# Optimization experiments

Hardware: AMD Instinct MI355X
Metric: run time of the kernel (lower is better)

## Reference

```python
import jax, jax.numpy as jnp
import numpy as np

NEG_INF = -1e6  # d2l masked_softmax fill value


def setup_inputs() -> dict:
    key = jax.random.key(0)
    kq, kk, kv, kl = jax.random.split(key, 4)
    n, s, d = 32, 2048, 64
    queries = jax.random.normal(kq, (n, s, d), dtype=jnp.float32)
    keys = jax.random.normal(kk, (n, s, d), dtype=jnp.float32)
    values = jax.random.normal(kv, (n, s, d), dtype=jnp.float32)
    valid_lens = jax.random.randint(kl, (n,), 1, s + 1, dtype=jnp.int32)
    return {"queries": queries, "keys": keys, "values": values, "valid_lens": valid_lens}


def reference(queries, keys, values, valid_lens):
    d = queries.shape[-1]
    # scores: [n, q, k]
    scores = jnp.einsum("nqd,nkd->nqk", queries, keys) / jnp.sqrt(jnp.float32(d))
    kv_len = scores.shape[-1]
    # masked_softmax: positions >= valid_len get NEG_INF before softmax
    mask = jnp.arange(kv_len, dtype=jnp.int32)[None, None, :] < valid_lens[:, None, None]
    scores = jnp.where(mask, scores, NEG_INF)
    attn = jax.nn.softmax(scores, axis=-1)
    # dropout rate 0.0 (inference) -> identity
    return jnp.einsum("nqk,nkd->nqd", attn, values)
```

## Files before the change

### kernel.cpp

```cpp
#include <hip/hip_runtime.h>
#include <hip/hip_bf16.h>


typedef short bf16x8 __attribute__((ext_vector_type(8)));
typedef float f32x4  __attribute__((ext_vector_type(4)));
typedef unsigned int u32;
typedef u32 u32x2 __attribute__((ext_vector_type(2)));
typedef u32 u32x4 __attribute__((ext_vector_type(4)));

#define SEQ 2048
#define DH 64
#define BK 64
#define LDSP 72
#define SCLQ 0.18033688011112042f

static __device__ __forceinline__ short f2bf(float f) {
    unsigned u = __float_as_uint(f);
    return (short)((u + 0x7FFFu + ((u >> 16) & 1u)) >> 16);
}
static __device__ __forceinline__ u32 pk2bf(float lo, float hi) {
    __hip_bfloat162 h = __float22bfloat162_rn(float2{lo, hi});
    return *(u32*)&h;
}

__global__ __launch_bounds__(256, 4)
void prepass(const float* __restrict__ K, const float* __restrict__ V,
             short* __restrict__ Kbf, short* __restrict__ Vt)
{
    __shared__ short T[DH][LDSP];

    const int tid  = threadIdx.x;
    const int wave = tid >> 6;
    const int lane = tid & 63;
    const int b  = blockIdx.x & 31;
    const int kt = blockIdx.x >> 5;
    const int k0 = kt * BK;
    const size_t bo = (size_t)b * SEQ * DH;

    const float* Ks = K + bo + (size_t)k0 * DH;
    u32* Kd = (u32*)(Kbf + bo + (size_t)k0 * DH);
    #pragma unroll
    for (int h = 0; h < 2; ++h) {
        const int c2 = tid + h * 256;
        f32x4 a = *(const f32x4*)(Ks + c2 * 8);
        f32x4 c = *(const f32x4*)(Ks + c2 * 8 + 4);
        u32x4 o;
        o[0] = pk2bf(a[0], a[1]); o[1] = pk2bf(a[2], a[3]);
        o[2] = pk2bf(c[0], c[1]); o[3] = pk2bf(c[2], c[3]);
        *(u32x4*)(Kd + c2 * 4) = o;
    }

    #pragma unroll
    for (int h = 0; h < 2; ++h) {
        const int d0 = wave * 8 + h * 32;
        const float* src = V + bo + (size_t)(k0 + lane) * DH + d0;
        f32x4 va = *(const f32x4*)(src);
        f32x4 vb = *(const f32x4*)(src + 4);
        #pragma unroll
        for (int j = 0; j < 4; ++j) {
            T[d0 + j][lane]     = f2bf(va[j]);
            T[d0 + 4 + j][lane] = f2bf(vb[j]);
        }
    }
    __syncthreads();

    short* Vd = Vt + (size_t)b * DH * SEQ;
    #pragma unroll
    for (int h = 0; h < 2; ++h) {
        const int c2 = tid + h * 256;
        const int d  = c2 >> 3;
        const int kc = (c2 & 7) * 8;
        *(bf16x8*)(Vd + (size_t)d * SEQ + k0 + kc) = *(const bf16x8*)(&T[d][kc]);
    }
}

template <bool PRE>
__global__ __launch_bounds__(256, 4)
void attn_fwd(const float* __restrict__ Q,
              const float* __restrict__ Kf, const float* __restrict__ Vf,
              const short* __restrict__ Kbf, const short* __restrict__ Vtg,
              const int* __restrict__ VL, float* __restrict__ O)
{
    __shared__ short Klds[BK][LDSP];
    __shared__ short Vt[DH][LDSP];
    __shared__ short Pw[4][16][LDSP];
    __shared__ int   Rsort[32];

    const int tid  = threadIdx.x;
    const int wave = tid >> 6;
    const int lane = tid & 63;
    const int g    = lane >> 4;
    const int l15  = lane & 15;

    if (tid < 32) {
        const int nv = (VL[tid] + BK - 1) >> 6;
        int rank = 0;
        for (int jj = 0; jj < 32; ++jj) {
            const int nj = (VL[jj] + BK - 1) >> 6;
            rank += (nj > nv) || (nj == nv && jj < tid);
        }
        Rsort[rank] = tid;
    }
    __syncthreads();

    const int jb = blockIdx.x & 255;
    const int sl = blockIdx.x >> 8;
    const int c8 = jb >> 5;
    const int qt = jb & 31;
    const int rk = (sl == 0) ? c8 : (sl == 1) ? (15 - c8)
                 : (sl == 2) ? (16 + c8) : (31 - c8);
    const int b  = Rsort[rk];

    const int vl  = VL[b];
    const int nkt = (vl + BK - 1) >> 6;

    const size_t bo = (size_t)b * SEQ * DH;
    const short* Kb = Kbf + bo;
    const short* Vb = Vtg + (size_t)b * DH * SEQ;
    const float* Kbf32 = Kf + bo;
    const float* Vbf32 = Vf + bo;

    const int qrow = qt * 64 + wave * 16 + l15;
    bf16x8 aq0, aq1;
    {
        const float* qp = Q + bo + (size_t)qrow * DH + g * 8;
        f32x4 q0 = *(const f32x4*)(qp);
        f32x4 q1 = *(const f32x4*)(qp + 4);
        f32x4 q2 = *(const f32x4*)(qp + 32);
        f32x4 q3 = *(const f32x4*)(qp + 36);
        #pragma unroll
        for (int j = 0; j < 4; ++j) {
            aq0[j]     = f2bf(q0[j] * SCLQ);
            aq0[j + 4] = f2bf(q1[j] * SCLQ);
            aq1[j]     = f2bf(q2[j] * SCLQ);
            aq1[j + 4] = f2bf(q3[j] * SCLQ);
        }
    }

    bf16x8 ones;
    #pragma unroll
    for (int j = 0; j < 8; ++j) ones[j] = (short)0x3F80;

    f32x4 oacc[4];
    #pragma unroll
    for (int i = 0; i < 4; ++i) oacc[i] = f32x4{0.f, 0.f, 0.f, 0.f};
    f32x4 lacc = f32x4{0.f, 0.f, 0.f, 0.f};

    bf16x8 kpre[2], vpre[2];
    f32x4 kpre32[4], vpre32[4];
    if (PRE) {
        #pragma unroll
        for (int h = 0; h < 2; ++h) {
            const int c2 = tid + h * 256;
            kpre[h] = *(const bf16x8*)(Kb + c2 * 8);
            vpre[h] = *(const bf16x8*)(Vb + (size_t)(c2 >> 3) * SEQ + ((c2 & 7) * 8));
        }
    } else {
        #pragma unroll
        for (int h = 0; h < 4; ++h) {
            const int cc = tid + h * 256;
            kpre32[h] = *(const f32x4*)(Kbf32 + (size_t)(cc >> 4) * DH + (cc & 15) * 4);
        }
        #pragma unroll
        for (int h = 0; h < 2; ++h) {
            const float* src = Vbf32 + (size_t)lane * DH + wave * 8 + h * 32;
            vpre32[2 * h]     = *(const f32x4*)(src);
            vpre32[2 * h + 1] = *(const f32x4*)(src + 4);
        }
    }

    for (int kt = 0; kt < nkt; ++kt) {
        const int k0 = kt * BK;

        if (PRE) {
            #pragma unroll
            for (int h = 0; h < 2; ++h) {
                const int c2 = tid + h * 256;
                *(bf16x8*)(&Klds[c2 >> 3][(c2 & 7) * 8]) = kpre[h];
                *(bf16x8*)(&Vt[c2 >> 3][(c2 & 7) * 8])   = vpre[h];
            }
        } else {
            #pragma unroll
            for (int h = 0; h < 4; ++h) {
                const int cc = tid + h * 256;
                u32x2 o;
                o[0] = pk2bf(kpre32[h][0], kpre32[h][1]);
                o[1] = pk2bf(kpre32[h][2], kpre32[h][3]);
                *(u32x2*)(&Klds[cc >> 4][(cc & 15) * 4]) = o;
            }
            #pragma unroll
            for (int h = 0; h < 2; ++h) {
                const int d0 = wave * 8 + h * 32;
                #pragma unroll
                for (int j = 0; j < 4; ++j) {
                    Vt[d0 + j][lane]     = f2bf(vpre32[2 * h][j]);
                    Vt[d0 + 4 + j][lane] = f2bf(vpre32[2 * h + 1][j]);
                }
            }
        }
        __syncthreads();

        if (kt + 1 < nkt) {
            const int kn = k0 + BK;
            if (PRE) {
                #pragma unroll
                for (int h = 0; h < 2; ++h) {
                    const int c2 = tid + h * 256;
                    kpre[h] = *(const bf16x8*)(Kb + (size_t)kn * DH + c2 * 8);
                    vpre[h] = *(const bf16x8*)(Vb + (size_t)(c2 >> 3) * SEQ + kn + ((c2 & 7) * 8));
                }
            } else {
                #pragma unroll
                for (int h = 0; h < 4; ++h) {
                    const int cc = tid + h * 256;
                    kpre32[h] = *(const f32x4*)(Kbf32 + (size_t)(kn + (cc >> 4)) * DH + (cc & 15) * 4);
                }
                #pragma unroll
                for (int h = 0; h < 2; ++h) {
                    const float* src = Vbf32 + (size_t)(kn + lane) * DH + wave * 8 + h * 32;
                    vpre32[2 * h]     = *(const f32x4*)(src);
                    vpre32[2 * h + 1] = *(const f32x4*)(src + 4);
                }
            }
        }

        f32x4 s[4];
        #pragma unroll
        for (int nb = 0; nb < 4; ++nb) {
            bf16x8 ak0 = *(const bf16x8*)(&Klds[nb * 16 + l15][g * 8]);
            bf16x8 ak1 = *(const bf16x8*)(&Klds[nb * 16 + l15][32 + g * 8]);
            f32x4 acc = f32x4{0.f, 0.f, 0.f, 0.f};
            acc = __builtin_amdgcn_mfma_f32_16x16x32_bf16(ak0, aq0, acc, 0, 0, 0);
            acc = __builtin_amdgcn_mfma_f32_16x16x32_bf16(ak1, aq1, acc, 0, 0, 0);
            s[nb] = acc;
        }

        if (k0 + BK <= vl) {
            #pragma unroll
            for (int nb = 0; nb < 4; ++nb)
                #pragma unroll
                for (int r = 0; r < 4; ++r)
                    s[nb][r] = __builtin_amdgcn_exp2f(s[nb][r]);
        } else {
            #pragma unroll
            for (int nb = 0; nb < 4; ++nb)
                #pragma unroll
                for (int r = 0; r < 4; ++r) {
                    const bool ok = (k0 + nb * 16 + g * 4 + r) < vl;
                    s[nb][r] = ok ? __builtin_amdgcn_exp2f(s[nb][r]) : 0.f;
                }
        }

        #pragma unroll
        for (int nb = 0; nb < 4; ++nb) {
            u32x2 pkv;
            pkv[0] = pk2bf(s[nb][0], s[nb][1]);
            pkv[1] = pk2bf(s[nb][2], s[nb][3]);
            *(u32x2*)(&Pw[wave][l15][nb * 16 + g * 4]) = pkv;
        }
        asm volatile("" ::: "memory");

        #pragma unroll
        for (int cc = 0; cc < 2; ++cc) {
            bf16x8 ap = *(const bf16x8*)(&Pw[wave][l15][cc * 32 + g * 8]);
            lacc = __builtin_amdgcn_mfma_f32_16x16x32_bf16(ap, ones, lacc, 0, 0, 0);
            #pragma unroll
            for (int db = 0; db < 4; ++db) {
                bf16x8 bv = *(const bf16x8*)(&Vt[db * 16 + l15][cc * 32 + g * 8]);
                oacc[db] = __builtin_amdgcn_mfma_f32_16x16x32_bf16(ap, bv, oacc[db], 0, 0, 0);
            }
        }
        __syncthreads();
    }

    #pragma unroll
    for (int r = 0; r < 4; ++r) {
        const float inv = 1.0f / lacc[r];
        const int row = qt * 64 + wave * 16 + g * 4 + r;
        #pragma unroll
        for (int db = 0; db < 4; ++db)
            O[bo + (size_t)row * DH + db * 16 + l15] = oacc[db][r] * inv;
    }
}

extern "C" void kernel_launch(void* const* d_in, const int* in_sizes, int n_in,
                              void* d_out, int out_size, void* d_ws, size_t ws_size,
                              hipStream_t stream) {
    const float* Q  = (const float*)d_in[0];
    const float* K  = (const float*)d_in[1];
    const float* V  = (const float*)d_in[2];
    const int*   VL = (const int*)d_in[3];
    float* O = (float*)d_out;

    const size_t nel = (size_t)32 * SEQ * DH;
    const size_t need = 2 * nel * sizeof(short);
    if (ws_size >= need) {
        short* Kbf = (short*)d_ws;
        short* Vt  = Kbf + nel;
        prepass<<<dim3(1024), dim3(256), 0, stream>>>(K, V, Kbf, Vt);
        attn_fwd<true><<<dim3(1024), dim3(256), 0, stream>>>(Q, K, V, Kbf, Vt, VL, O);
    } else {
        attn_fwd<false><<<dim3(1024), dim3(256), 0, stream>>>(Q, K, V, nullptr, nullptr, VL, O);
    }
}
```

Measured before the change: 128.3 us.

## Switch attention to 32x32 MFMA with split-K wave groups and register P

Rewrites the attention kernel to use 32x32x16 bf16 MFMAs. Waves are split into two query groups and two key-tile groups, and each key-group pair processes alternate 64-key tiles with double-buffered LDS. The softmax P tile now stays in registers and is re-laid out with v_permlane32_swap, which removes the LDS round trip. Partial outputs and row sums from the two key groups are combined through LDS at the end. The change also raises register pressure (launch bounds drop to 2 blocks) and sets wave priority around the MFMA section.

Result: slower. 132.1 us (+3.0%).

```diff
diff --git a/kernel.cpp b/kernel.cpp
--- a/kernel.cpp
+++ b/kernel.cpp
@@ -4,6 +4,7 @@
 
 typedef short bf16x8 __attribute__((ext_vector_type(8)));
 typedef float f32x4  __attribute__((ext_vector_type(4)));
+typedef float f32x16 __attribute__((ext_vector_type(16)));
 typedef unsigned int u32;
 typedef u32 u32x2 __attribute__((ext_vector_type(2)));
 typedef u32 u32x4 __attribute__((ext_vector_type(4)));
@@ -21,6 +22,9 @@
 static __device__ __forceinline__ u32 pk2bf(float lo, float hi) {
     __hip_bfloat162 h = __float22bfloat162_rn(float2{lo, hi});
     return *(u32*)&h;
+}
+static __device__ __forceinline__ void pl32swap(u32& a, u32& b) {
+    asm volatile("v_permlane32_swap_b32 %0, %1" : "+v"(a), "+v"(b));
 }
 
 __global__ __launch_bounds__(256, 4)
@@ -75,22 +79,24 @@
 }
 
 template <bool PRE>
-__global__ __launch_bounds__(256, 4)
+__global__ __launch_bounds__(256, 2)
 void attn_fwd(const float* __restrict__ Q,
               const float* __restrict__ Kf, const float* __restrict__ Vf,
               const short* __restrict__ Kbf, const short* __restrict__ Vtg,
               const int* __restrict__ VL, float* __restrict__ O)
 {
-    __shared__ short Klds[BK][LDSP];
-    __shared__ short Vt[DH][LDSP];
-    __shared__ short Pw[4][16][LDSP];
-    __shared__ int   Rsort[32];
+    __shared__ __align__(16) short Klds[2][BK][LDSP];
+    __shared__ __align__(16) short Vt[2][DH][LDSP];
+    __shared__ int Rsort[32];
 
     const int tid  = threadIdx.x;
     const int wave = tid >> 6;
     const int lane = tid & 63;
-    const int g    = lane >> 4;
-    const int l15  = lane & 15;
+    const int qg   = wave & 1;
+    const int kg   = wave >> 1;
+    const int hi   = lane >> 5;
+    const int l31  = lane & 31;
+    const int pt   = (qg << 6) | lane;
 
     if (tid < 32) {
         const int nv = (VL[tid] + BK - 1) >> 6;
@@ -111,29 +117,29 @@
                  : (sl == 2) ? (16 + c8) : (31 - c8);
     const int b  = Rsort[rk];
 
-    const int vl  = VL[b];
-    const int nkt = (vl + BK - 1) >> 6;
+    const int vl   = VL[b];
+    const int nkt  = (vl + BK - 1) >> 6;
+    const int nkt2 = (nkt + 1) >> 1;
 
     const size_t bo = (size_t)b * SEQ * DH;
     const short* Kb = Kbf + bo;
     const short* Vb = Vtg + (size_t)b * DH * SEQ;
-    const float* Kbf32 = Kf + bo;
-    const float* Vbf32 = Vf + bo;
-
-    const int qrow = qt * 64 + wave * 16 + l15;
-    bf16x8 aq0, aq1;
+    const float* Kb32 = Kf + bo;
+    const float* Vb32 = Vf + bo;
+
+    const int qrow = qt * 64 + qg * 32 + l31;
+    bf16x8 aq[4];
     {
-        const float* qp = Q + bo + (size_t)qrow * DH + g * 8;
-        f32x4 q0 = *(const f32x4*)(qp);
-        f32x4 q1 = *(const f32x4*)(qp + 4);
-        f32x4 q2 = *(const f32x4*)(qp + 32);
-        f32x4 q3 = *(const f32x4*)(qp + 36);
+        const float* qp = Q + bo + (size_t)qrow * DH + hi * 8;
         #pragma unroll
-        for (int j = 0; j < 4; ++j) {
-            aq0[j]     = f2bf(q0[j] * SCLQ);
-            aq0[j + 4] = f2bf(q1[j] * SCLQ);
-            aq1[j]     = f2bf(q2[j] * SCLQ);
-            aq1[j + 4] = f2bf(q3[j] * SCLQ);
+        for (int st = 0; st < 4; ++st) {
+            f32x4 a = *(const f32x4*)(qp + st * 16);
+            f32x4 c = *(const f32x4*)(qp + st * 16 + 4);
+            #pragma unroll
+            for (int j = 0; j < 4; ++j) {
+                aq[st][j]     = f2bf(a[j] * SCLQ);
+                aq[st][j + 4] = f2bf(c[j] * SCLQ);
+            }
         }
     }
 
@@ -141,145 +147,153 @@
     #pragma unroll
     for (int j = 0; j < 8; ++j) ones[j] = (short)0x3F80;
 
-    f32x4 oacc[4];
-    #pragma unroll
-    for (int i = 0; i < 4; ++i) oacc[i] = f32x4{0.f, 0.f, 0.f, 0.f};
-    f32x4 lacc = f32x4{0.f, 0.f, 0.f, 0.f};
-
-    bf16x8 kpre[2], vpre[2];
-    f32x4 kpre32[4], vpre32[4];
-    if (PRE) {
-        #pragma unroll
-        for (int h = 0; h < 2; ++h) {
-            const int c2 = tid + h * 256;
-            kpre[h] = *(const bf16x8*)(Kb + c2 * 8);
-            vpre[h] = *(const bf16x8*)(Vb + (size_t)(c2 >> 3) * SEQ + ((c2 & 7) * 8));
-        }
-    } else {
+    f32x16 oacc0, oacc1, lacc;
+    #pragma unroll
+    for (int i = 0; i < 16; ++i) { oacc0[i] = 0.f; oacc1[i] = 0.f; lacc[i] = 0.f; }
+
+    bf16x8 kpre[4], vpre[4];
+    if (PRE && kg < nkt) {
+        const size_t k0p = (size_t)kg * BK;
         #pragma unroll
         for (int h = 0; h < 4; ++h) {
-            const int cc = tid + h * 256;
-            kpre32[h] = *(const f32x4*)(Kbf32 + (size_t)(cc >> 4) * DH + (cc & 15) * 4);
-        }
+            const int c = pt + h * 128;
+            kpre[h] = *(const bf16x8*)(Kb + k0p * DH + c * 8);
+            vpre[h] = *(const bf16x8*)(Vb + (size_t)(c >> 3) * SEQ + k0p + (c & 7) * 8);
+        }
+    }
+
+    int kt = kg;
+    for (int it = 0; it < nkt2; ++it, kt += 2) {
+        const bool act = (kt < nkt);
+        const int k0 = kt * BK;
+
+        if (act) {
+            if (PRE) {
+                #pragma unroll
+                for (int h = 0; h < 4; ++h) {
+                    const int c = pt + h * 128;
+                    *(bf16x8*)(&Klds[kg][c >> 3][(c & 7) * 8]) = kpre[h];
+                    *(bf16x8*)(&Vt[kg][c >> 3][(c & 7) * 8])   = vpre[h];
+                }
+            } else {
+                #pragma unroll
+                for (int h = 0; h < 4; ++h) {
+                    const int c = pt + h * 128;
+                    const float* ks = Kb32 + (size_t)(k0 + (c >> 3)) * DH + (c & 7) * 8;
+                    f32x4 a = *(const f32x4*)ks;
+                    f32x4 d = *(const f32x4*)(ks + 4);
+                    u32x4 o;
+                    o[0] = pk2bf(a[0], a[1]); o[1] = pk2bf(a[2], a[3]);
+                    o[2] = pk2bf(d[0], d[1]); o[3] = pk2bf(d[2], d[3]);
+                    *(u32x4*)(&Klds[kg][c >> 3][(c & 7) * 8]) = o;
+                }
+                #pragma unroll
+                for (int h = 0; h < 4; ++h) {
+                    const int d0 = qg * 32 + h * 8;
+                    const float* vs = Vb32 + (size_t)(k0 + lane) * DH + d0;
+                    f32x4 a = *(const f32x4*)vs;
+                    f32x4 d = *(const f32x4*)(vs + 4);
+                    #pragma unroll
+                    for (int j = 0; j < 4; ++j) {
+                        Vt[kg][d0 + j][lane]     = f2bf(a[j]);
+                        Vt[kg][d0 + 4 + j][lane] = f2bf(d[j]);
+                    }
+                }
+            }
+        }
+        __syncthreads();
+
+        if (PRE && kt + 2 < nkt) {
+            const size_t kn = (size_t)(k0 + 2 * BK);
+            #pragma unroll
+            for (int h = 0; h < 4; ++h) {
+                const int c = pt + h * 128;
+                kpre[h] = *(const bf16x8*)(Kb + kn * DH + c * 8);
+                vpre[h] = *(const bf16x8*)(Vb + (size_t)(c >> 3) * SEQ + kn + (c & 7) * 8);
+            }
+        }
+
+        if (act) {
+            __builtin_amdgcn_s_setprio(1);
+            f32x16 s0, s1;
+            #pragma unroll
+            for (int i = 0; i < 16; ++i) { s0[i] = 0.f; s1[i] = 0.f; }
+            #pragma unroll
+            for (int st = 0; st < 4; ++st) {
+                bf16x8 a0 = *(const bf16x8*)(&Klds[kg][l31][st * 16 + hi * 8]);
+                bf16x8 a1 = *(const bf16x8*)(&Klds[kg][32 + l31][st * 16 + hi * 8]);
+                s0 = __builtin_amdgcn_mfma_f32_32x32x16_bf16(a0, aq[st], s0, 0, 0, 0);
+                s1 = __builtin_amdgcn_mfma_f32_32x32x16_bf16(a1, aq[st], s1, 0, 0, 0);
+            }
+
+            if (k0 + BK <= vl) {
+                #pragma unroll
+                for (int r = 0; r < 16; ++r) {
+                    s0[r] = __builtin_amdgcn_exp2f(s0[r]);
+                    s1[r] = __builtin_amdgcn_exp2f(s1[r]);
+                }
+            } else {
+                #pragma unroll
+                for (int r = 0; r < 16; ++r) {
+                    const int krow = k0 + (r & 3) + 8 * (r >> 2) + 4 * hi;
+                    s0[r] = (krow < vl)      ? __builtin_amdgcn_exp2f(s0[r]) : 0.f;
+                    s1[r] = (krow + 32 < vl) ? __builtin_amdgcn_exp2f(s1[r]) : 0.f;
+                }
+            }
+
+            u32 pk0[8], pk1[8];
+            #pragma unroll
+            for (int i = 0; i < 8; ++i) {
+                pk0[i] = pk2bf(s0[2 * i], s0[2 * i + 1]);
+                pk1[i] = pk2bf(s1[2 * i], s1[2 * i + 1]);
+            }
+
+            bf16x8 ap[4];
+            #pragma unroll
+            for (int t = 0; t < 2; ++t) {
+                u32 x0 = pk0[4 * t], x1 = pk0[4 * t + 1];
+                u32 x2 = pk0[4 * t + 2], x3 = pk0[4 * t + 3];
+                pl32swap(x0, x2); pl32swap(x1, x3);
+                u32x4 w; w[0] = x0; w[1] = x1; w[2] = x2; w[3] = x3;
+                ap[t] = *(bf16x8*)&w;
+                u32 y0 = pk1[4 * t], y1 = pk1[4 * t + 1];
+                u32 y2 = pk1[4 * t + 2], y3 = pk1[4 * t + 3];
+                pl32swap(y0, y2); pl32swap(y1, y3);
+                u32x4 v; v[0] = y0; v[1] = y1; v[2] = y2; v[3] = y3;
+                ap[2 + t] = *(bf16x8*)&v;
+            }
+
+            #pragma unroll
+            for (int ks = 0; ks < 4; ++ks) {
+                lacc = __builtin_amdgcn_mfma_f32_32x32x16_bf16(ap[ks], ones, lacc, 0, 0, 0);
+                bf16x8 b0 = *(const bf16x8*)(&Vt[kg][l31][ks * 16 + hi * 8]);
+                bf16x8 b1 = *(const bf16x8*)(&Vt[kg][32 + l31][ks * 16 + hi * 8]);
+                oacc0 = __builtin_amdgcn_mfma_f32_32x32x16_bf16(ap[ks], b0, oacc0, 0, 0, 0);
+                oacc1 = __builtin_amdgcn_mfma_f32_32x32x16_bf16(ap[ks], b1, oacc1, 0, 0, 0);
+            }
+            __builtin_amdgcn_s_setprio(0);
+        }
+        __syncthreads();
+    }
+
+    float* red = (qg ? (float*)&Vt[0][0][0] : (float*)&Klds[0][0][0]) + lane * 52;
+    if (kg == 1) {
+        *(f32x16*)(red)      = oacc0;
+        *(f32x16*)(red + 16) = oacc1;
+        *(f32x16*)(red + 32) = lacc;
+    }
+    __syncthreads();
+    if (kg == 0) {
+        f32x16 po0 = *(const f32x16*)(red);
+        f32x16 po1 = *(const f32x16*)(red + 16);
+        f32x16 pl  = *(const f32x16*)(red + 32);
         #pragma unroll
-        for (int h = 0; h < 2; ++h) {
-            const float* src = Vbf32 + (size_t)lane * DH + wave * 8 + h * 32;
-            vpre32[2 * h]     = *(const f32x4*)(src);
-            vpre32[2 * h + 1] = *(const f32x4*)(src + 4);
-        }
-    }
-
-    for (int kt = 0; kt < nkt; ++kt) {
-        const int k0 = kt * BK;
-
-        if (PRE) {
-            #pragma unroll
-            for (int h = 0; h < 2; ++h) {
-                const int c2 = tid + h * 256;
-                *(bf16x8*)(&Klds[c2 >> 3][(c2 & 7) * 8]) = kpre[h];
-                *(bf16x8*)(&Vt[c2 >> 3][(c2 & 7) * 8])   = vpre[h];
-            }
-        } else {
-            #pragma unroll
-            for (int h = 0; h < 4; ++h) {
-                const int cc = tid + h * 256;
-                u32x2 o;
-                o[0] = pk2bf(kpre32[h][0], kpre32[h][1]);
-                o[1] = pk2bf(kpre32[h][2], kpre32[h][3]);
-                *(u32x2*)(&Klds[cc >> 4][(cc & 15) * 4]) = o;
-            }
-            #pragma unroll
-            for (int h = 0; h < 2; ++h) {
-                const int d0 = wave * 8 + h * 32;
-                #pragma unroll
-                for (int j = 0; j < 4; ++j) {
-                    Vt[d0 + j][lane]     = f2bf(vpre32[2 * h][j]);
-                    Vt[d0 + 4 + j][lane] = f2bf(vpre32[2 * h + 1][j]);
-                }
-            }
-        }
-        __syncthreads();
-
-        if (kt + 1 < nkt) {
-            const int kn = k0 + BK;
-            if (PRE) {
-                #pragma unroll
-                for (int h = 0; h < 2; ++h) {
-                    const int c2 = tid + h * 256;
-                    kpre[h] = *(const bf16x8*)(Kb + (size_t)kn * DH + c2 * 8);
-                    vpre[h] = *(const bf16x8*)(Vb + (size_t)(c2 >> 3) * SEQ + kn + ((c2 & 7) * 8));
-                }
-            } else {
-                #pragma unroll
-                for (int h = 0; h < 4; ++h) {
-                    const int cc = tid + h * 256;
-                    kpre32[h] = *(const f32x4*)(Kbf32 + (size_t)(kn + (cc >> 4)) * DH + (cc & 15) * 4);
-                }
-                #pragma unroll
-                for (int h = 0; h < 2; ++h) {
-                    const float* src = Vbf32 + (size_t)(kn + lane) * DH + wave * 8 + h * 32;
-                    vpre32[2 * h]     = *(const f32x4*)(src);
-                    vpre32[2 * h + 1] = *(const f32x4*)(src + 4);
-                }
-            }
-        }
-
-        f32x4 s[4];
-        #pragma unroll
-        for (int nb = 0; nb < 4; ++nb) {
-            bf16x8 ak0 = *(const bf16x8*)(&Klds[nb * 16 + l15][g * 8]);
-            bf16x8 ak1 = *(const bf16x8*)(&Klds[nb * 16 + l15][32 + g * 8]);
-            f32x4 acc = f32x4{0.f, 0.f, 0.f, 0.f};
-            acc = __builtin_amdgcn_mfma_f32_16x16x32_bf16(ak0, aq0, acc, 0, 0, 0);
-            acc = __builtin_amdgcn_mfma_f32_16x16x32_bf16(ak1, aq1, acc, 0, 0, 0);
-            s[nb] = acc;
-        }
-
-        if (k0 + BK <= vl) {
-            #pragma unroll
-            for (int nb = 0; nb < 4; ++nb)
-                #pragma unroll
-                for (int r = 0; r < 4; ++r)
-                    s[nb][r] = __builtin_amdgcn_exp2f(s[nb][r]);
-        } else {
-            #pragma unroll
-            for (int nb = 0; nb < 4; ++nb)
-                #pragma unroll
-                for (int r = 0; r < 4; ++r) {
-                    const bool ok = (k0 + nb * 16 + g * 4 + r) < vl;
-                    s[nb][r] = ok ? __builtin_amdgcn_exp2f(s[nb][r]) : 0.f;
-                }
-        }
-
-        #pragma unroll
-        for (int nb = 0; nb < 4; ++nb) {
-            u32x2 pkv;
-            pkv[0] = pk2bf(s[nb][0], s[nb][1]);
-            pkv[1] = pk2bf(s[nb][2], s[nb][3]);
-            *(u32x2*)(&Pw[wave][l15][nb * 16 + g * 4]) = pkv;
-        }
-        asm volatile("" ::: "memory");
-
-        #pragma unroll
-        for (int cc = 0; cc < 2; ++cc) {
-            bf16x8 ap = *(const bf16x8*)(&Pw[wave][l15][cc * 32 + g * 8]);
-            lacc = __builtin_amdgcn_mfma_f32_16x16x32_bf16(ap, ones, lacc, 0, 0, 0);
-            #pragma unroll
-            for (int db = 0; db < 4; ++db) {
-                bf16x8 bv = *(const bf16x8*)(&Vt[db * 16 + l15][cc * 32 + g * 8]);
-                oacc[db] = __builtin_amdgcn_mfma_f32_16x16x32_bf16(ap, bv, oacc[db], 0, 0, 0);
-            }
-        }
-        __syncthreads();
-    }
-
-    #pragma unroll
-    for (int r = 0; r < 4; ++r) {
-        const float inv = 1.0f / lacc[r];
-        const int row = qt * 64 + wave * 16 + g * 4 + r;
-        #pragma unroll
-        for (int db = 0; db < 4; ++db)
-            O[bo + (size_t)row * DH + db * 16 + l15] = oacc[db][r] * inv;
+        for (int r = 0; r < 16; ++r) {
+            const float inv = 1.0f / (lacc[r] + pl[r]);
+            const int row = qt * 64 + qg * 32 + (r & 3) + 8 * (r >> 2) + 4 * hi;
+            O[bo + (size_t)row * DH + l31]      = (oacc0[r] + po0[r]) * inv;
+            O[bo + (size_t)row * DH + 32 + l31] = (oacc1[r] + po1[r]) * inv;
+        }
     }
 }
 
```
